# Performance work log

Hardware: AMD Instinct MI355X
Metric: run time of the kernel (lower is better)

## Reference

```python
import jax, jax.numpy as jnp
import numpy as np

B, N, D = 4, 4096, 256
HEADS, OUT = 4, 64


def setup_inputs() -> dict:
    key = jax.random.key(0)
    ks = jax.random.split(key, 6)
    features = jax.random.normal(ks[0], (B, N, D), dtype=jnp.float32)
    adj = jax.random.randint(ks[1], (B, N, N), 0, 2).astype(jnp.float32)
    s_fc = 1.0 / np.sqrt(D)
    W_fc = jax.random.uniform(ks[2], (OUT * HEADS, D), jnp.float32, -s_fc, s_fc)
    b_fc = jnp.zeros((OUT * HEADS,), jnp.float32)
    s_a = 1.0 / np.sqrt(2 * OUT * HEADS)
    W_attn = jax.random.uniform(ks[3], (HEADS, 2 * OUT * HEADS), jnp.float32, -s_a, s_a)
    b_attn = jax.random.uniform(ks[4], (HEADS,), jnp.float32, -s_a, s_a)
    return {"features": features, "adj": adj, "W_fc": W_fc, "b_fc": b_fc,
            "W_attn": W_attn, "b_attn": b_attn}


def reference(features, adj, W_fc, b_fc, W_attn, b_attn):
    b, n, d = features.shape
    heads = W_attn.shape[0]
    out = W_fc.shape[0] // heads
    # h: [b, n, heads, out]  (fc output reshaped head-major, matching torch .view)
    h = (features @ W_fc.T + b_fc).reshape(b, n, heads, out)
    # attn linear on concat([h_src, h_dst]) flattened as (heads, [src_out | dst_out]),
    # then mean over the `heads` output dim -> score decomposes additively:
    # e[b,i,j] = src[b,j] + dst[b,i] + mean(b_attn)
    Wa = W_attn.reshape(heads, heads, 2 * out)  # [k_out, h_in, 2*out]
    W_src = Wa[:, :, :out].mean(axis=0)   # [heads, out]
    W_dst = Wa[:, :, out:].mean(axis=0)   # [heads, out]
    src = jnp.einsum('bjho,ho->bj', h, W_src)  # depends on source node j
    dst = jnp.einsum('biho,ho->bi', h, W_dst)  # depends on dest node i
    scores = dst[:, :, None] + src[:, None, :] + b_attn.mean()  # [b, n, n]
    scores = scores + (1.0 - adj) * (-1e9)
    alpha = jax.nn.softmax(scores, axis=2)  # softmax over source nodes j
    # torch einsum 'bijk,bjkl->bijl' broadcasts attn's size-1 k against heads,
    # so aggregation uses sum over heads of h; final .mean(dim=2) divides by n.
    h_sum = h.sum(axis=2)  # [b, n, out]
    out_feat = jnp.einsum('bij,bjl->bil', alpha, h_sum) / n
    return out_feat
```

## Files before the change

### kernel.cpp

```cpp
#include <hip/hip_runtime.h>
#include <stdint.h>
#include <math.h>


#define Bz   4
#define Nn   4096
#define Dd   256
#define OUTd 64
#define GTR  80

typedef float    f32x4   __attribute__((ext_vector_type(4)));
typedef __fp16   fp16x2  __attribute__((ext_vector_type(2)));
typedef _Float16 half8_t __attribute__((ext_vector_type(8)));

__device__ inline half8_t cvt8(float4 a, float4 b) {
  union { fp16x2 h2[4]; half8_t h8; } r;
  r.h2[0] = __builtin_amdgcn_cvt_pkrtz(a.x, a.y);
  r.h2[1] = __builtin_amdgcn_cvt_pkrtz(a.z, a.w);
  r.h2[2] = __builtin_amdgcn_cvt_pkrtz(b.x, b.y);
  r.h2[3] = __builtin_amdgcn_cvt_pkrtz(b.z, b.w);
  return r.h8;
}

__global__ __launch_bounds__(256) void k_prep_ws(const float* __restrict__ W_attn,
                                                 const float* __restrict__ b_fc,
                                                 float* __restrict__ w_s,
                                                 float* __restrict__ hb,
                                                 float* __restrict__ sb) {
  __shared__ float ws_sh[256];
  __shared__ float red[64];
  int t = threadIdx.x;
  int h = t >> 6, l = t & 63;
  float s = 0.f;
  for (int k = 0; k < 4; ++k) s += W_attn[k * 512 + h * 128 + l];
  s *= 0.25f;
  ws_sh[t] = s;
  w_s[t] = s;
  if (t < 64) {
    float hbv = 0.f;
    for (int hh = 0; hh < 4; ++hh) hbv += b_fc[hh * 64 + t];
    hb[t] = hbv;
  }
  __syncthreads();
  if (t < 64) {
    float p = 0.f;
    for (int k = 0; k < 4; ++k) p += b_fc[t + 64 * k] * ws_sh[t + 64 * k];
    red[t] = p;
  }
  __syncthreads();
  if (t == 0) {
    float a = 0.f;
    for (int i = 0; i < 64; ++i) a += red[i];
    *sb = a;
  }
}

__global__ __launch_bounds__(256) void k_prep_ut(const float* __restrict__ W_fc,
                                                 const float* __restrict__ w_s,
                                                 _Float16* __restrict__ Ut) {
  int l = blockIdx.x, d = threadIdx.x;
  float v;
  if (l < 64) {
    v = W_fc[l * 256 + d] + W_fc[(64 + l) * 256 + d] +
        W_fc[(128 + l) * 256 + d] + W_fc[(192 + l) * 256 + d];
  } else {
    v = 0.f;
    for (int ho = 0; ho < 256; ++ho) v += W_fc[ho * 256 + d] * w_s[ho];
  }
  Ut[l * 256 + d] = (_Float16)v;
}

__global__ __launch_bounds__(256) void k_feat(const float* __restrict__ feat,
                                              const _Float16* __restrict__ Ut,
                                              const float* __restrict__ hb,
                                              const float* __restrict__ sb,
                                              _Float16* __restrict__ Gt) {
  const int b = blockIdx.y;
  const int tid = threadIdx.x;
  const int lane = tid & 63;
  const int wv = tid >> 6;
  const int ln15 = lane & 15;
  const int quad = lane >> 4;
  const int j = blockIdx.x * 64 + wv * 16 + ln15;

  const float* frow = feat + ((size_t)b * Nn + j) * Dd + quad * 8;
  f32x4 acc0 = {0,0,0,0}, acc1 = {0,0,0,0}, acc2 = {0,0,0,0}, acc3 = {0,0,0,0}, acc4 = {0,0,0,0};

  #pragma unroll
  for (int d0 = 0; d0 < Dd; d0 += 32) {
    float4 F0 = *(const float4*)(frow + d0);
    float4 F1 = *(const float4*)(frow + d0 + 4);
    half8_t bf = cvt8(F0, F1);
    const _Float16* up = Ut + (size_t)ln15 * Dd + d0 + quad * 8;
    acc0 = __builtin_amdgcn_mfma_f32_16x16x32_f16(*(const half8_t*)(up + 0 * 16 * Dd), bf, acc0, 0, 0, 0);
    acc1 = __builtin_amdgcn_mfma_f32_16x16x32_f16(*(const half8_t*)(up + 1 * 16 * Dd), bf, acc1, 0, 0, 0);
    acc2 = __builtin_amdgcn_mfma_f32_16x16x32_f16(*(const half8_t*)(up + 2 * 16 * Dd), bf, acc2, 0, 0, 0);
    acc3 = __builtin_amdgcn_mfma_f32_16x16x32_f16(*(const half8_t*)(up + 3 * 16 * Dd), bf, acc3, 0, 0, 0);
    acc4 = __builtin_amdgcn_mfma_f32_16x16x32_f16(*(const half8_t*)(up + 4 * 16 * Dd), bf, acc4, 0, 0, 0);
  }
  float srcv = __shfl(acc4[0], ln15) + sb[0];
  float p = expf(srcv);
  _Float16* gb = Gt + (size_t)b * GTR * Nn;
  #pragma unroll
  for (int r = 0; r < 4; ++r) {
    int lb = quad * 4 + r;
    gb[(size_t)(0  + lb) * Nn + j] = (_Float16)((acc0[r] + hb[0  + lb]) * p);
    gb[(size_t)(16 + lb) * Nn + j] = (_Float16)((acc1[r] + hb[16 + lb]) * p);
    gb[(size_t)(32 + lb) * Nn + j] = (_Float16)((acc2[r] + hb[32 + lb]) * p);
    gb[(size_t)(48 + lb) * Nn + j] = (_Float16)((acc3[r] + hb[48 + lb]) * p);
  }
  if (quad == 0) gb[(size_t)64 * Nn + j] = (_Float16)p;
}

__global__ __launch_bounds__(256) void k_agg(const float* __restrict__ adj,
                                             const _Float16* __restrict__ Gt,
                                             float* __restrict__ out) {
  const int b = blockIdx.y;
  const int tid = threadIdx.x;
  const int lane = tid & 63;
  const int wv = tid >> 6;
  const int ln15 = lane & 15;
  const int quad = lane >> 4;
  const int i0 = blockIdx.x * 64 + wv * 16;

  const float* arow = adj + ((size_t)b * Nn + (i0 + ln15)) * (size_t)Nn + quad * 8;
  const _Float16* g0 = Gt + ((size_t)b * GTR + ln15) * Nn + quad * 8;
  const _Float16* g1 = g0 + (size_t)16 * Nn;
  const _Float16* g2 = g0 + (size_t)32 * Nn;
  const _Float16* g3 = g0 + (size_t)48 * Nn;
  const _Float16* g4 = g0 + (size_t)64 * Nn;

  f32x4 acc0 = {0,0,0,0}, acc1 = {0,0,0,0}, acc2 = {0,0,0,0}, acc3 = {0,0,0,0}, acc4 = {0,0,0,0};

  for (int k0 = 0; k0 < Nn; k0 += 64) {
    float4 A0 = *(const float4*)(arow + k0);
    float4 A1 = *(const float4*)(arow + k0 + 4);
    float4 A2 = *(const float4*)(arow + k0 + 32);
    float4 A3 = *(const float4*)(arow + k0 + 36);
    half8_t b00 = *(const half8_t*)(g0 + k0);
    half8_t b01 = *(const half8_t*)(g1 + k0);
    half8_t b02 = *(const half8_t*)(g2 + k0);
    half8_t b03 = *(const half8_t*)(g3 + k0);
    half8_t b04 = *(const half8_t*)(g4 + k0);
    half8_t b10 = *(const half8_t*)(g0 + k0 + 32);
    half8_t b11 = *(const half8_t*)(g1 + k0 + 32);
    half8_t b12 = *(const half8_t*)(g2 + k0 + 32);
    half8_t b13 = *(const half8_t*)(g3 + k0 + 32);
    half8_t b14 = *(const half8_t*)(g4 + k0 + 32);
    half8_t aF0 = cvt8(A0, A1);
    half8_t aF1 = cvt8(A2, A3);
    acc0 = __builtin_amdgcn_mfma_f32_16x16x32_f16(aF0, b00, acc0, 0, 0, 0);
    acc1 = __builtin_amdgcn_mfma_f32_16x16x32_f16(aF0, b01, acc1, 0, 0, 0);
    acc2 = __builtin_amdgcn_mfma_f32_16x16x32_f16(aF0, b02, acc2, 0, 0, 0);
    acc3 = __builtin_amdgcn_mfma_f32_16x16x32_f16(aF0, b03, acc3, 0, 0, 0);
    acc4 = __builtin_amdgcn_mfma_f32_16x16x32_f16(aF0, b04, acc4, 0, 0, 0);
    acc0 = __builtin_amdgcn_mfma_f32_16x16x32_f16(aF1, b10, acc0, 0, 0, 0);
    acc1 = __builtin_amdgcn_mfma_f32_16x16x32_f16(aF1, b11, acc1, 0, 0, 0);
    acc2 = __builtin_amdgcn_mfma_f32_16x16x32_f16(aF1, b12, acc2, 0, 0, 0);
    acc3 = __builtin_amdgcn_mfma_f32_16x16x32_f16(aF1, b13, acc3, 0, 0, 0);
    acc4 = __builtin_amdgcn_mfma_f32_16x16x32_f16(aF1, b14, acc4, 0, 0, 0);
  }

  float den0 = __shfl(acc4[0], lane & 48);
  float den1 = __shfl(acc4[1], lane & 48);
  float den2 = __shfl(acc4[2], lane & 48);
  float den3 = __shfl(acc4[3], lane & 48);
  const float invn = 1.0f / (float)Nn;
  float* orow = out + ((size_t)b * Nn + i0) * OUTd;
  #pragma unroll
  for (int r = 0; r < 4; ++r) {
    float d = (r == 0) ? den0 : (r == 1) ? den1 : (r == 2) ? den2 : den3;
    float rd = invn / d;
    int ir = quad * 4 + r;
    orow[(size_t)ir * OUTd + 0  + ln15] = acc0[r] * rd;
    orow[(size_t)ir * OUTd + 16 + ln15] = acc1[r] * rd;
    orow[(size_t)ir * OUTd + 32 + ln15] = acc2[r] * rd;
    orow[(size_t)ir * OUTd + 48 + ln15] = acc3[r] * rd;
  }
}

extern "C" void kernel_launch(void* const* d_in, const int* in_sizes, int n_in,
                              void* d_out, int out_size, void* d_ws, size_t ws_size,
                              hipStream_t stream) {
  const float* feat   = (const float*)d_in[0];
  const float* adj    = (const float*)d_in[1];
  const float* W_fc   = (const float*)d_in[2];
  const float* b_fc   = (const float*)d_in[3];
  const float* W_attn = (const float*)d_in[4];
  (void)d_in[5];
  float* out = (float*)d_out;

  char* ws = (char*)d_ws;
  _Float16* Gt = (_Float16*)ws;
  _Float16* Ut = (_Float16*)(ws + 2621440);
  float*    w_s = (float*)(ws + 2621440 + 40960);
  float*    hb  = (float*)(ws + 2621440 + 40960 + 1024);
  float*    sb  = (float*)(ws + 2621440 + 40960 + 1024 + 256);

  k_prep_ws<<<1, 256, 0, stream>>>(W_attn, b_fc, w_s, hb, sb);
  k_prep_ut<<<65, 256, 0, stream>>>(W_fc, w_s, Ut);
  k_feat<<<dim3(64, 4), 256, 0, stream>>>(feat, Ut, hb, sb, Gt);
  k_agg<<<dim3(64, 4), 256, 0, stream>>>(adj, Gt, out);
}
```

Baseline: 414.2 us.

## Split aggregation over K into four chunks with a separate reduction kernel

The aggregation kernel is split along the source-node dimension into four chunks via blockIdx.z, which raises the grid from 256 to 1024 blocks so the GPU's compute units are better filled. Each chunk writes partial numerators and the softmax denominator to a workspace buffer. A new finalize kernel sums the partials and applies the normalization and 1/N scaling. The cost is an extra kernel launch plus a round trip of partial results through global memory.

```diff
diff --git a/kernel.cpp b/kernel.cpp
--- a/kernel.cpp
+++ b/kernel.cpp
@@ -8,6 +8,8 @@
 #define Dd   256
 #define OUTd 64
 #define GTR  80
+#define KSPLIT 4
+#define KCH  (Nn / KSPLIT)
 
 typedef float    f32x4   __attribute__((ext_vector_type(4)));
 typedef __fp16   fp16x2  __attribute__((ext_vector_type(2)));
@@ -114,8 +116,9 @@
 
 __global__ __launch_bounds__(256) void k_agg(const float* __restrict__ adj,
                                              const _Float16* __restrict__ Gt,
-                                             float* __restrict__ out) {
+                                             float* __restrict__ part) {
   const int b = blockIdx.y;
+  const int z = blockIdx.z;
   const int tid = threadIdx.x;
   const int lane = tid & 63;
   const int wv = tid >> 6;
@@ -132,7 +135,8 @@
 
   f32x4 acc0 = {0,0,0,0}, acc1 = {0,0,0,0}, acc2 = {0,0,0,0}, acc3 = {0,0,0,0}, acc4 = {0,0,0,0};
 
-  for (int k0 = 0; k0 < Nn; k0 += 64) {
+  const int kbeg = z * KCH, kend = kbeg + KCH;
+  for (int k0 = kbeg; k0 < kend; k0 += 64) {
     float4 A0 = *(const float4*)(arow + k0);
     float4 A1 = *(const float4*)(arow + k0 + 4);
     float4 A2 = *(const float4*)(arow + k0 + 32);
@@ -161,22 +165,31 @@
     acc4 = __builtin_amdgcn_mfma_f32_16x16x32_f16(aF1, b14, acc4, 0, 0, 0);
   }
 
-  float den0 = __shfl(acc4[0], lane & 48);
-  float den1 = __shfl(acc4[1], lane & 48);
-  float den2 = __shfl(acc4[2], lane & 48);
-  float den3 = __shfl(acc4[3], lane & 48);
-  const float invn = 1.0f / (float)Nn;
-  float* orow = out + ((size_t)b * Nn + i0) * OUTd;
+  float* prow = part + (((size_t)z * Bz + b) * Nn + i0) * 80;
   #pragma unroll
   for (int r = 0; r < 4; ++r) {
-    float d = (r == 0) ? den0 : (r == 1) ? den1 : (r == 2) ? den2 : den3;
-    float rd = invn / d;
     int ir = quad * 4 + r;
-    orow[(size_t)ir * OUTd + 0  + ln15] = acc0[r] * rd;
-    orow[(size_t)ir * OUTd + 16 + ln15] = acc1[r] * rd;
-    orow[(size_t)ir * OUTd + 32 + ln15] = acc2[r] * rd;
-    orow[(size_t)ir * OUTd + 48 + ln15] = acc3[r] * rd;
-  }
+    prow[(size_t)ir * 80 + 0  + ln15] = acc0[r];
+    prow[(size_t)ir * 80 + 16 + ln15] = acc1[r];
+    prow[(size_t)ir * 80 + 32 + ln15] = acc2[r];
+    prow[(size_t)ir * 80 + 48 + ln15] = acc3[r];
+    prow[(size_t)ir * 80 + 64 + ln15] = acc4[r];
+  }
+}
+
+__global__ __launch_bounds__(256) void k_fin(const float* __restrict__ part,
+                                             float* __restrict__ out) {
+  const int t = threadIdx.x;
+  const int rl = t >> 6, l = t & 63;
+  const size_t row = (size_t)blockIdx.x * 4 + rl;
+  float num = 0.f, den = 0.f;
+  #pragma unroll
+  for (int z = 0; z < KSPLIT; ++z) {
+    const float* p = part + ((size_t)z * Bz * Nn + row) * 80;
+    num += p[l];
+    den += p[64];
+  }
+  out[row * OUTd + l] = num / den * (1.0f / (float)Nn);
 }
 
 extern "C" void kernel_launch(void* const* d_in, const int* in_sizes, int n_in,
@@ -196,9 +209,11 @@
   float*    w_s = (float*)(ws + 2621440 + 40960);
   float*    hb  = (float*)(ws + 2621440 + 40960 + 1024);
   float*    sb  = (float*)(ws + 2621440 + 40960 + 1024 + 256);
+  float*    part = (float*)(ws + 2664448);
 
   k_prep_ws<<<1, 256, 0, stream>>>(W_attn, b_fc, w_s, hb, sb);
   k_prep_ut<<<65, 256, 0, stream>>>(W_fc, w_s, Ut);
   k_feat<<<dim3(64, 4), 256, 0, stream>>>(feat, Ut, hb, sb, Gt);
-  k_agg<<<dim3(64, 4), 256, 0, stream>>>(adj, Gt, out);
-}
+  k_agg<<<dim3(64, 4, KSPLIT), 256, 0, stream>>>(adj, Gt, part);
+  k_fin<<<Bz * Nn / 4, 256, 0, stream>>>(part, out);
+}
```

After: 425.9 us. 2.8% more time.
